# Kernel tuning notes

Measured on AMD Instinct MI355X. Metric: run time of the kernel, lower is better.

The kernel has to match this reference:

```python
import jax, jax.numpy as jnp
import numpy as np

N_REF = 4

def setup_inputs() -> dict:
    key = jax.random.key(0)
    ks = jax.random.split(key, 6)
    B, C, H, W = 4, 256, 64, 64
    s = 1.0 / np.sqrt(C)
    return {
        'x': jax.random.normal(ks[0], (B, C, H, W), jnp.float32),
        'Wq': jax.random.normal(ks[1], (C, C), jnp.float32) * s,
        'bq': jnp.zeros((C,), jnp.float32),
        'Wk': jax.random.normal(ks[2], (C, C), jnp.float32) * s,
        'bk': jnp.zeros((C,), jnp.float32),
        'Wv': jax.random.normal(ks[3], (C, C), jnp.float32) * s,
        'bv': jnp.zeros((C,), jnp.float32),
        'Woff': jax.random.normal(ks[4], (2 * N_REF, C), jnp.float32) * s,
        'boff': jnp.zeros((2 * N_REF,), jnp.float32),
    }

def _proj(x, W, b):
    # 1x1 conv == channel-mixing linear: [B,C,H,W] -> [B,O,H,W]
    return jnp.einsum('oc,bchw->bohw', W, x) + b[None, :, None, None]

def reference(x, Wq, bq, Wk, bk, Wv, bv, Woff, boff):
    B, C, H, W = x.shape
    n = N_REF
    HW = H * W
    Q = _proj(x, Wq, bq)
    K = _proj(x, Wk, bk)
    V = _proj(x, Wv, bv)
    offsets = _proj(Q, Woff, boff).reshape(B, n, 2, H, W)
    grid_h, grid_w = jnp.meshgrid(jnp.arange(H), jnp.arange(W), indexing='ij')
    ref_x = jnp.clip(jnp.round(grid_w[None, None] + offsets[:, :, 0]).astype(jnp.int32), 0, W - 1)
    ref_y = jnp.clip(jnp.round(grid_h[None, None] + offsets[:, :, 1]).astype(jnp.int32), 0, H - 1)
    ref_idx = (ref_y * W + ref_x).reshape(B, n, HW)          # [B,n,HW]
    K_flat = K.reshape(B, C, HW)
    V_flat = V.reshape(B, C, HW)
    # gather along spatial dim -> [B,C,n,HW]
    idx = ref_idx[:, None, :, :]                              # [B,1,n,HW]
    K_g = jnp.take_along_axis(K_flat[:, :, None, :], idx, axis=3)
    V_g = jnp.take_along_axis(V_flat[:, :, None, :], idx, axis=3)
    Q_flat = Q.reshape(B, C, HW)
    attn = jnp.einsum('bch,bcnh->bnh', Q_flat, K_g)
    attn = jax.nn.softmax(attn, axis=1)
    out = jnp.einsum('bnh,bcnh->bch', attn, V_g)
    return out.reshape(B, C, H, W)
```

## Files before the change

### kernel.cpp

```cpp
#include <hip/hip_runtime.h>
#include <math.h>

#define B_DIM   4
#define C_DIM   256
#define H_DIM   64
#define W_DIM   64
#define HW_DIM  4096
#define NPIX    (B_DIM * HW_DIM)
#define NREF    4

typedef unsigned short u16;
typedef __attribute__((ext_vector_type(4))) unsigned short u16x4;
typedef __attribute__((ext_vector_type(8))) unsigned short u16x8;
typedef __attribute__((ext_vector_type(8))) short bf16x8;
typedef __attribute__((ext_vector_type(4))) float f32x4;

__device__ __forceinline__ u16 bf16_rne(float f) {
    unsigned u = __float_as_uint(f);
    u = u + 0x7FFFu + ((u >> 16) & 1u);
    return (u16)(u >> 16);
}
__device__ __forceinline__ float bf16_tof(u16 h) {
    return __uint_as_float(((unsigned)h) << 16);
}
__device__ __forceinline__ void gload16(const void* g, void* l) {
    __builtin_amdgcn_global_load_lds(
        (const __attribute__((address_space(1))) void*)g,
        (__attribute__((address_space(3))) void*)l, 16, 0, 0);
}

__global__ __launch_bounds__(256) void prep_kernel(
    const float* __restrict__ Wq, const float* __restrict__ bq,
    const float* __restrict__ Woff, const float* __restrict__ boff,
    const float* __restrict__ Wk, const float* __restrict__ Wv,
    double* __restrict__ Weffp, double* __restrict__ beff,
    u16* __restrict__ Bswh, u16* __restrict__ Bswl)
{
    const int bx = blockIdx.x;
    const int t  = threadIdx.x;

    if (bx < 32) {
        const int j  = bx >> 2;
        const int q  = bx & 3;
        const int o0 = q * 64;
        double s0 = 0, s1 = 0, s2 = 0, s3 = 0;
        for (int o = o0; o < o0 + 64; o += 4) {
            s0 += (double)Woff[j * C_DIM + o + 0] * (double)Wq[(size_t)(o + 0) * C_DIM + t];
            s1 += (double)Woff[j * C_DIM + o + 1] * (double)Wq[(size_t)(o + 1) * C_DIM + t];
            s2 += (double)Woff[j * C_DIM + o + 2] * (double)Wq[(size_t)(o + 2) * C_DIM + t];
            s3 += (double)Woff[j * C_DIM + o + 3] * (double)Wq[(size_t)(o + 3) * C_DIM + t];
        }
        Weffp[(size_t)(q * 8 + j) * C_DIM + t] = (s0 + s1) + (s2 + s3);

        if (q == 0) {
            __shared__ double red[256];
            red[t] = (double)Woff[j * C_DIM + t] * (double)bq[t];
            __syncthreads();
            for (int st = 128; st > 0; st >>= 1) {
                if (t < st) red[t] += red[t + st];
                __syncthreads();
            }
            if (t == 0) beff[j] = red[0] + (double)boff[j];
        }
    } else {
        const int T     = bx - 32;
        const int kt    = T & 3;
        const int ntile = (T >> 2) & 1;
        const int mat   = T >> 3;
        const float* Wm = (mat == 0) ? Wq : (mat == 1) ? Wk : Wv;
        const int n0 = ntile * 128, k0 = kt * 64;
        u16* dh = Bswh + (size_t)T * 8192;
        u16* dl = Bswl + (size_t)T * 8192;
#pragma unroll
        for (int it = 0; it < 4; ++it) {
            const int s   = it * 256 + t;
            const int row = s >> 3;
            const int ch  = s & 7;
            const int kk  = k0 + (ch ^ (row & 7)) * 8;
            const float4 w0 = *(const float4*)(Wm + (size_t)(n0 + row) * C_DIM + kk);
            const float4 w1 = *(const float4*)(Wm + (size_t)(n0 + row) * C_DIM + kk + 4);
            u16x8 hv, lv;
            hv[0] = bf16_rne(w0.x); lv[0] = bf16_rne(w0.x - bf16_tof(hv[0]));
            hv[1] = bf16_rne(w0.y); lv[1] = bf16_rne(w0.y - bf16_tof(hv[1]));
            hv[2] = bf16_rne(w0.z); lv[2] = bf16_rne(w0.z - bf16_tof(hv[2]));
            hv[3] = bf16_rne(w0.w); lv[3] = bf16_rne(w0.w - bf16_tof(hv[3]));
            hv[4] = bf16_rne(w1.x); lv[4] = bf16_rne(w1.x - bf16_tof(hv[4]));
            hv[5] = bf16_rne(w1.y); lv[5] = bf16_rne(w1.y - bf16_tof(hv[5]));
            hv[6] = bf16_rne(w1.z); lv[6] = bf16_rne(w1.z - bf16_tof(hv[6]));
            hv[7] = bf16_rne(w1.w); lv[7] = bf16_rne(w1.w - bf16_tof(hv[7]));
            *(u16x8*)(dh + (size_t)s * 8) = hv;
            *(u16x8*)(dl + (size_t)s * 8) = lv;
        }
    }
}

__global__ __launch_bounds__(256) void xsplit_kernel(
    const float* __restrict__ x, const double* __restrict__ Weffp,
    u16* __restrict__ xh, u16* __restrict__ xl, double* __restrict__ part)
{
    __shared__ float  tile[64][65];
    __shared__ double wf[8][64];
    const int b   = blockIdx.z;
    const int cy  = blockIdx.y;
    const int c0  = cy * 64;
    const int hw0 = blockIdx.x * 64;
    const int t   = threadIdx.x;
    const int r4  = t >> 6;
    const int col = t & 63;

#pragma unroll
    for (int i = 0; i < 16; ++i) {
        const int row = i * 4 + r4;
        tile[row][col] = x[((size_t)b * C_DIM + c0 + row) * HW_DIM + hw0 + col];
    }
#pragma unroll
    for (int d = t; d < 512; d += 256) {
        const int jj = d >> 6, cc = d & 63;
        ((double*)wf)[d] = Weffp[(size_t)(0 + jj) * C_DIM + c0 + cc]
                         + Weffp[(size_t)(8 + jj) * C_DIM + c0 + cc]
                         + Weffp[(size_t)(16 + jj) * C_DIM + c0 + cc]
                         + Weffp[(size_t)(24 + jj) * C_DIM + c0 + cc];
    }
    __syncthreads();

#pragma unroll
    for (int i = 0; i < 16; ++i) {
        const int hwr = i * 4 + r4;
        const float v = tile[col][hwr];
        const u16 h = bf16_rne(v);
        const float lo = v - bf16_tof(h);
        const size_t o = ((size_t)b * HW_DIM + hw0 + hwr) * C_DIM + c0 + col;
        xh[o] = h;
        xl[o] = bf16_rne(lo);
    }

    const int p = col, g = r4;
    double a0 = 0, a1 = 0;
    for (int c = 0; c < 64; ++c) {
        const double xv = (double)tile[c][p];
        a0 += wf[2 * g][c] * xv;
        a1 += wf[2 * g + 1][c] * xv;
    }
    const int pix = b * HW_DIM + hw0 + p;
    part[(size_t)(cy * 8 + 2 * g) * NPIX + pix]     = a0;
    part[(size_t)(cy * 8 + 2 * g + 1) * NPIX + pix] = a1;
}

__global__ __launch_bounds__(256) void idx_kernel(
    const double* __restrict__ part, const double* __restrict__ beff,
    int* __restrict__ idx_buf)
{
    const int pix = blockIdx.x * 256 + threadIdx.x;
    const int hw  = pix & (HW_DIM - 1);
    const int h   = hw >> 6;
    const int w   = hw & 63;

    double o[8];
#pragma unroll
    for (int j = 0; j < 8; ++j)
        o[j] = part[(size_t)(0 + j) * NPIX + pix] + part[(size_t)(8 + j) * NPIX + pix]
             + part[(size_t)(16 + j) * NPIX + pix] + part[(size_t)(24 + j) * NPIX + pix]
             + beff[j];

    int r[NREF];
#pragma unroll
    for (int n = 0; n < NREF; ++n) {
        const float ox = (float)o[2 * n];
        const float oy = (float)o[2 * n + 1];
        int rx = (int)rintf((float)w + ox);
        int ry = (int)rintf((float)h + oy);
        rx = min(max(rx, 0), W_DIM - 1);
        ry = min(max(ry, 0), H_DIM - 1);
        r[n] = ry * W_DIM + rx;
    }
    int4 outv; outv.x = r[0]; outv.y = r[1]; outv.z = r[2]; outv.w = r[3];
    *(int4*)(idx_buf + (size_t)pix * 4) = outv;
}

__global__ __launch_bounds__(256) void qkv_mfma(
    const u16* __restrict__ xh, const u16* __restrict__ xl,
    const u16* __restrict__ Bswh, const u16* __restrict__ Bswl,
    const float* __restrict__ bq, const float* __restrict__ bk,
    const float* __restrict__ bv,
    float* __restrict__ Qt, float* __restrict__ Kt, float* __restrict__ Vt)
{
    const int mat   = blockIdx.z;
    const int ntile = blockIdx.y;
    const int m0    = blockIdx.x * 64;
    const int n0    = ntile * 128;
    const bool three = (mat != 2);
    const float* bm = (mat == 0) ? bq : (mat == 1) ? bk : bv;
    float*      Out = (mat == 0) ? Qt : (mat == 1) ? Kt : Vt;

    __shared__ u16 lds[24576];
    u16* Ah = lds;
    u16* Al = lds + 4096;
    u16* Bh = lds + 8192;
    u16* Bl = lds + 16384;

    const int t    = threadIdx.x;
    const int lane = t & 63;
    const int wv   = t >> 6;
    const int wm   = (wv >> 1) * 32;
    const int wn   = (wv & 1) * 64;

    f32x4 acc[2][4] = {};

    for (int kt = 0; kt < 4; ++kt) {
        const int k0 = kt * 64;
        const size_t Tb = (size_t)((mat * 2 + ntile) * 4 + kt) * 8192;

#pragma unroll
        for (int it = 0; it < 2; ++it) {
            const int s   = it * 256 + t;
            const int row = s >> 3;
            const int sch = (s & 7) ^ (row & 7);
            const size_t goff = (size_t)(m0 + row) * C_DIM + k0 + sch * 8;
            gload16(xh + goff, (char*)Ah + s * 16);
            if (three) gload16(xl + goff, (char*)Al + s * 16);
        }
#pragma unroll
        for (int it = 0; it < 4; ++it) {
            const int s = it * 256 + t;
            gload16(Bswh + Tb + (size_t)s * 8, (char*)Bh + s * 16);
            if (three) gload16(Bswl + Tb + (size_t)s * 8, (char*)Bl + s * 16);
        }
        __syncthreads();

#pragma unroll
        for (int ks = 0; ks < 2; ++ks) {
            bf16x8 afh[2], afl[2], bfh[4], bfl[4];
#pragma unroll
            for (int mt = 0; mt < 2; ++mt) {
                const int row = wm + mt * 16 + (lane & 15);
                const int ch  = (ks * 4 + (lane >> 4)) ^ (row & 7);
                const int off = row * 128 + ch * 16;
                afh[mt] = *(const bf16x8*)((const char*)Ah + off);
                if (three) afl[mt] = *(const bf16x8*)((const char*)Al + off);
            }
#pragma unroll
            for (int nt = 0; nt < 4; ++nt) {
                const int row = wn + nt * 16 + (lane & 15);
                const int ch  = (ks * 4 + (lane >> 4)) ^ (row & 7);
                const int off = row * 128 + ch * 16;
                bfh[nt] = *(const bf16x8*)((const char*)Bh + off);
                if (three) bfl[nt] = *(const bf16x8*)((const char*)Bl + off);
            }
#pragma unroll
            for (int mt = 0; mt < 2; ++mt)
#pragma unroll
                for (int nt = 0; nt < 4; ++nt) {
                    acc[mt][nt] = __builtin_amdgcn_mfma_f32_16x16x32_bf16(afh[mt], bfh[nt], acc[mt][nt], 0, 0, 0);
                    if (three) {
                        acc[mt][nt] = __builtin_amdgcn_mfma_f32_16x16x32_bf16(afh[mt], bfl[nt], acc[mt][nt], 0, 0, 0);
                        acc[mt][nt] = __builtin_amdgcn_mfma_f32_16x16x32_bf16(afl[mt], bfh[nt], acc[mt][nt], 0, 0, 0);
                    }
                }
        }
        __syncthreads();
    }

    const int col = lane & 15;
    const int rg  = (lane >> 4) * 4;
#pragma unroll
    for (int nt = 0; nt < 4; ++nt) {
        const int n = n0 + wn + nt * 16 + col;
        const float bias = bm[n];
#pragma unroll
        for (int mt = 0; mt < 2; ++mt) {
            const int m = m0 + wm + mt * 16 + rg;
#pragma unroll
            for (int r = 0; r < 4; ++r)
                Out[(size_t)(m + r) * C_DIM + n] = acc[mt][nt][r] + bias;
        }
    }
}

__global__ __launch_bounds__(1024) void attn_kernel(
    const float* __restrict__ Qt,
    const float* __restrict__ Kt,
    const float* __restrict__ Vt,
    const int*   __restrict__ idx_buf,
    float* __restrict__ out)
{
    __shared__ float trans[16][260];

    const int t    = threadIdx.x;
    const int wave = t >> 6;
    const int lane = t & 63;

    const int pix0 = blockIdx.x * 16;
    const int b    = pix0 / HW_DIM;
    const int hw   = (pix0 % HW_DIM) + wave;
    const int pix  = b * HW_DIM + hw;

    const float* qrow = Qt + (size_t)pix * C_DIM;
    float q[4];
    *(float4*)q = *(const float4*)(qrow + lane * 4);

    const int4 iv = *(const int4*)(idx_buf + (size_t)pix * 4);
    int idx[NREF] = {iv.x, iv.y, iv.z, iv.w};

    float logit[NREF];
#pragma unroll
    for (int n = 0; n < NREF; ++n) {
        const float* krow = Kt + ((size_t)b * HW_DIM + idx[n]) * C_DIM;
        float4 kv = *(const float4*)(krow + lane * 4);
        float lp = fmaf(q[3], kv.w, fmaf(q[2], kv.z, fmaf(q[1], kv.y, q[0] * kv.x)));
#pragma unroll
        for (int off = 1; off < 64; off <<= 1) lp += __shfl_xor(lp, off);
        logit[n] = lp;
    }

    float mx = fmaxf(fmaxf(logit[0], logit[1]), fmaxf(logit[2], logit[3]));
    float e[NREF], s = 0.0f;
#pragma unroll
    for (int n = 0; n < NREF; ++n) { e[n] = expf(logit[n] - mx); s += e[n]; }
    float wgt[NREF];
#pragma unroll
    for (int n = 0; n < NREF; ++n) wgt[n] = e[n] / s;

    float o4[4] = {0.f, 0.f, 0.f, 0.f};
#pragma unroll
    for (int n = 0; n < NREF; ++n) {
        const float* vrow = Vt + ((size_t)b * HW_DIM + idx[n]) * C_DIM;
        float4 vv = *(const float4*)(vrow + lane * 4);
        o4[0] = fmaf(wgt[n], vv.x, o4[0]);
        o4[1] = fmaf(wgt[n], vv.y, o4[1]);
        o4[2] = fmaf(wgt[n], vv.z, o4[2]);
        o4[3] = fmaf(wgt[n], vv.w, o4[3]);
    }

    *(float4*)&trans[wave][lane * 4] = *(float4*)o4;
    __syncthreads();

    float* ob = out + (size_t)b * C_DIM * HW_DIM + (pix0 % HW_DIM);
    const int px = t & 15;
#pragma unroll
    for (int cc = 0; cc < C_DIM; cc += 64) {
        const int c = cc + (t >> 4);
        ob[(size_t)c * HW_DIM + px] = trans[px][c];
    }
}

extern "C" void kernel_launch(void* const* d_in, const int* in_sizes, int n_in,
                              void* d_out, int out_size, void* d_ws, size_t ws_size,
                              hipStream_t stream) {
    const float* x    = (const float*)d_in[0];
    const float* Wq   = (const float*)d_in[1];
    const float* bq   = (const float*)d_in[2];
    const float* Wk   = (const float*)d_in[3];
    const float* bk   = (const float*)d_in[4];
    const float* Wv   = (const float*)d_in[5];
    const float* bv   = (const float*)d_in[6];
    const float* Woff = (const float*)d_in[7];
    const float* boff = (const float*)d_in[8];
    float* out = (float*)d_out;

    char* ws = (char*)d_ws;
    float*  Kt    = (float*)ws;
    float*  Vt    = (float*)(ws + (size_t)16 * 1024 * 1024);
    float*  Qt    = (float*)(ws + (size_t)32 * 1024 * 1024);
    u16*    xh    = (u16*)  (ws + (size_t)48 * 1024 * 1024);
    u16*    xl    = (u16*)  (ws + (size_t)56 * 1024 * 1024);
    char*   aux   = ws + (size_t)64 * 1024 * 1024;
    double* Weffp = (double*)(aux);
    double* beff  = (double*)(aux + 64 * 1024);
    int*    idxb  = (int*)   (aux + 128 * 1024);
    u16*    Bswh  = (u16*)   (aux + 512 * 1024);
    u16*    Bswl  = (u16*)   (aux + 1024 * 1024);
    double* part  = (double*)(aux + 2 * 1024 * 1024);

    prep_kernel<<<dim3(56), dim3(256), 0, stream>>>(
        Wq, bq, Woff, boff, Wk, Wv, Weffp, beff, Bswh, Bswl);
    xsplit_kernel<<<dim3(HW_DIM / 64, C_DIM / 64, B_DIM), dim3(256), 0, stream>>>(
        x, Weffp, xh, xl, part);
    idx_kernel<<<dim3(NPIX / 256), dim3(256), 0, stream>>>(part, beff, idxb);
    qkv_mfma<<<dim3(NPIX / 64, 2, 3), dim3(256), 0, stream>>>(
        xh, xl, Bswh, Bswl, bq, bk, bv, Qt, Kt, Vt);
    attn_kernel<<<dim3(NPIX / 16), dim3(1024), 0, stream>>>(
        Qt, Kt, Vt, idxb, out);
}
```

Baseline: 62.79 us.

## Fold Wq into K projection to eliminate the Q GEMM

```diff
diff --git a/kernel.cpp b/kernel.cpp
--- a/kernel.cpp
+++ b/kernel.cpp
@@ -8,6 +8,7 @@
 #define HW_DIM  4096
 #define NPIX    (B_DIM * HW_DIM)
 #define NREF    4
+#define NJ      10
 
 typedef unsigned short u16;
 typedef __attribute__((ext_vector_type(4))) unsigned short u16x4;
@@ -29,68 +30,95 @@
         (__attribute__((address_space(3))) void*)l, 16, 0, 0);
 }
 
-__global__ __launch_bounds__(256) void prep_kernel(
+__global__ __launch_bounds__(256) void prep1_kernel(
     const float* __restrict__ Wq, const float* __restrict__ bq,
+    const float* __restrict__ Wk, const float* __restrict__ bk,
     const float* __restrict__ Woff, const float* __restrict__ boff,
-    const float* __restrict__ Wk, const float* __restrict__ Wv,
     double* __restrict__ Weffp, double* __restrict__ beff,
-    u16* __restrict__ Bswh, u16* __restrict__ Bswl)
+    double* __restrict__ Mt)
 {
     const int bx = blockIdx.x;
     const int t  = threadIdx.x;
 
-    if (bx < 32) {
+    if (bx < 4 * NJ) {
         const int j  = bx >> 2;
         const int q  = bx & 3;
         const int o0 = q * 64;
+        const float* Avec = (j < 8) ? (Woff + j * C_DIM) : ((j == 8) ? bq : bk);
+        const float* Bmat = (j == 8) ? Wk : Wq;
         double s0 = 0, s1 = 0, s2 = 0, s3 = 0;
         for (int o = o0; o < o0 + 64; o += 4) {
-            s0 += (double)Woff[j * C_DIM + o + 0] * (double)Wq[(size_t)(o + 0) * C_DIM + t];
-            s1 += (double)Woff[j * C_DIM + o + 1] * (double)Wq[(size_t)(o + 1) * C_DIM + t];
-            s2 += (double)Woff[j * C_DIM + o + 2] * (double)Wq[(size_t)(o + 2) * C_DIM + t];
-            s3 += (double)Woff[j * C_DIM + o + 3] * (double)Wq[(size_t)(o + 3) * C_DIM + t];
-        }
-        Weffp[(size_t)(q * 8 + j) * C_DIM + t] = (s0 + s1) + (s2 + s3);
-
-        if (q == 0) {
+            s0 += (double)Avec[o + 0] * (double)Bmat[(size_t)(o + 0) * C_DIM + t];
+            s1 += (double)Avec[o + 1] * (double)Bmat[(size_t)(o + 1) * C_DIM + t];
+            s2 += (double)Avec[o + 2] * (double)Bmat[(size_t)(o + 2) * C_DIM + t];
+            s3 += (double)Avec[o + 3] * (double)Bmat[(size_t)(o + 3) * C_DIM + t];
+        }
+        Weffp[(size_t)(q * NJ + j) * C_DIM + t] = (s0 + s1) + (s2 + s3);
+
+        if (q == 0 && j <= 8) {
             __shared__ double red[256];
-            red[t] = (double)Woff[j * C_DIM + t] * (double)bq[t];
+            red[t] = (j < 8) ? (double)Woff[j * C_DIM + t] * (double)bq[t]
+                             : (double)bq[t] * (double)bk[t];
             __syncthreads();
             for (int st = 128; st > 0; st >>= 1) {
                 if (t < st) red[t] += red[t + st];
                 __syncthreads();
             }
-            if (t == 0) beff[j] = red[0] + (double)boff[j];
+            if (t == 0) beff[j] = (j < 8) ? red[0] + (double)boff[j] : red[0];
         }
     } else {
-        const int T     = bx - 32;
-        const int kt    = T & 3;
-        const int ntile = (T >> 2) & 1;
-        const int mat   = T >> 3;
-        const float* Wm = (mat == 0) ? Wq : (mat == 1) ? Wk : Wv;
-        const int n0 = ntile * 128, k0 = kt * 64;
-        u16* dh = Bswh + (size_t)T * 8192;
-        u16* dl = Bswl + (size_t)T * 8192;
-#pragma unroll
-        for (int it = 0; it < 4; ++it) {
-            const int s   = it * 256 + t;
-            const int row = s >> 3;
-            const int ch  = s & 7;
-            const int kk  = k0 + (ch ^ (row & 7)) * 8;
-            const float4 w0 = *(const float4*)(Wm + (size_t)(n0 + row) * C_DIM + kk);
-            const float4 w1 = *(const float4*)(Wm + (size_t)(n0 + row) * C_DIM + kk + 4);
-            u16x8 hv, lv;
-            hv[0] = bf16_rne(w0.x); lv[0] = bf16_rne(w0.x - bf16_tof(hv[0]));
-            hv[1] = bf16_rne(w0.y); lv[1] = bf16_rne(w0.y - bf16_tof(hv[1]));
-            hv[2] = bf16_rne(w0.z); lv[2] = bf16_rne(w0.z - bf16_tof(hv[2]));
-            hv[3] = bf16_rne(w0.w); lv[3] = bf16_rne(w0.w - bf16_tof(hv[3]));
-            hv[4] = bf16_rne(w1.x); lv[4] = bf16_rne(w1.x - bf16_tof(hv[4]));
-            hv[5] = bf16_rne(w1.y); lv[5] = bf16_rne(w1.y - bf16_tof(hv[5]));
-            hv[6] = bf16_rne(w1.z); lv[6] = bf16_rne(w1.z - bf16_tof(hv[6]));
-            hv[7] = bf16_rne(w1.w); lv[7] = bf16_rne(w1.w - bf16_tof(hv[7]));
-            *(u16x8*)(dh + (size_t)s * 8) = hv;
-            *(u16x8*)(dl + (size_t)s * 8) = lv;
-        }
+        const int c = bx - 4 * NJ;
+        __shared__ float wqcol[256];
+        wqcol[t] = Wq[(size_t)t * C_DIM + c];
+        __syncthreads();
+        double a0 = 0, a1 = 0, a2 = 0, a3 = 0;
+        for (int o = 0; o < C_DIM; o += 4) {
+            a0 += (double)wqcol[o + 0] * (double)Wk[(size_t)(o + 0) * C_DIM + t];
+            a1 += (double)wqcol[o + 1] * (double)Wk[(size_t)(o + 1) * C_DIM + t];
+            a2 += (double)wqcol[o + 2] * (double)Wk[(size_t)(o + 2) * C_DIM + t];
+            a3 += (double)wqcol[o + 3] * (double)Wk[(size_t)(o + 3) * C_DIM + t];
+        }
+        Mt[(size_t)c * C_DIM + t] = (a0 + a1) + (a2 + a3);
+    }
+}
+
+__global__ __launch_bounds__(256) void prep2_kernel(
+    const double* __restrict__ Mt, const float* __restrict__ Wv,
+    u16* __restrict__ Bswh, u16* __restrict__ Bswl)
+{
+    const int T     = blockIdx.x;
+    const int kt    = T & 3;
+    const int ntile = (T >> 2) & 1;
+    const int mat   = T >> 3;
+    const int n0 = ntile * 128, k0 = kt * 64;
+    const int t  = threadIdx.x;
+    u16* dh = Bswh + (size_t)T * 8192;
+    u16* dl = Bswl + (size_t)T * 8192;
+
+#pragma unroll
+    for (int it = 0; it < 4; ++it) {
+        const int s   = it * 256 + t;
+        const int row = s >> 3;
+        const int ch  = s & 7;
+        const int kk  = k0 + (ch ^ (row & 7)) * 8;
+        float v[8];
+        if (mat == 0) {
+            const double* src = Mt + (size_t)(n0 + row) * C_DIM + kk;
+#pragma unroll
+            for (int i = 0; i < 8; ++i) v[i] = (float)src[i];
+        } else {
+            const float* src = Wv + (size_t)(n0 + row) * C_DIM + kk;
+#pragma unroll
+            for (int i = 0; i < 8; ++i) v[i] = src[i];
+        }
+        u16x8 hv, lv;
+#pragma unroll
+        for (int i = 0; i < 8; ++i) {
+            hv[i] = bf16_rne(v[i]);
+            lv[i] = bf16_rne(v[i] - bf16_tof(hv[i]));
+        }
+        *(u16x8*)(dh + (size_t)s * 8) = hv;
+        if (mat == 0) *(u16x8*)(dl + (size_t)s * 8) = lv;
     }
 }
 
@@ -99,7 +127,7 @@
     u16* __restrict__ xh, u16* __restrict__ xl, double* __restrict__ part)
 {
     __shared__ float  tile[64][65];
-    __shared__ double wf[8][64];
+    __shared__ double wf[NJ][64];
     const int b   = blockIdx.z;
     const int cy  = blockIdx.y;
     const int c0  = cy * 64;
@@ -113,13 +141,12 @@
         const int row = i * 4 + r4;
         tile[row][col] = x[((size_t)b * C_DIM + c0 + row) * HW_DIM + hw0 + col];
     }
-#pragma unroll
-    for (int d = t; d < 512; d += 256) {
+    for (int d = t; d < NJ * 64; d += 256) {
         const int jj = d >> 6, cc = d & 63;
-        ((double*)wf)[d] = Weffp[(size_t)(0 + jj) * C_DIM + c0 + cc]
-                         + Weffp[(size_t)(8 + jj) * C_DIM + c0 + cc]
-                         + Weffp[(size_t)(16 + jj) * C_DIM + c0 + cc]
-                         + Weffp[(size_t)(24 + jj) * C_DIM + c0 + cc];
+        ((double*)wf)[d] = Weffp[(size_t)(0 * NJ + jj) * C_DIM + c0 + cc]
+                         + Weffp[(size_t)(1 * NJ + jj) * C_DIM + c0 + cc]
+                         + Weffp[(size_t)(2 * NJ + jj) * C_DIM + c0 + cc]
+                         + Weffp[(size_t)(3 * NJ + jj) * C_DIM + c0 + cc];
     }
     __syncthreads();
 
@@ -135,20 +162,22 @@
     }
 
     const int p = col, g = r4;
-    double a0 = 0, a1 = 0;
+    double a0 = 0, a1 = 0, a2 = 0;
     for (int c = 0; c < 64; ++c) {
         const double xv = (double)tile[c][p];
         a0 += wf[2 * g][c] * xv;
         a1 += wf[2 * g + 1][c] * xv;
+        if (g < 2) a2 += wf[8 + g][c] * xv;
     }
     const int pix = b * HW_DIM + hw0 + p;
-    part[(size_t)(cy * 8 + 2 * g) * NPIX + pix]     = a0;
-    part[(size_t)(cy * 8 + 2 * g + 1) * NPIX + pix] = a1;
+    part[(size_t)(cy * NJ + 2 * g) * NPIX + pix]     = a0;
+    part[(size_t)(cy * NJ + 2 * g + 1) * NPIX + pix] = a1;
+    if (g < 2) part[(size_t)(cy * NJ + 8 + g) * NPIX + pix] = a2;
 }
 
 __global__ __launch_bounds__(256) void idx_kernel(
     const double* __restrict__ part, const double* __restrict__ beff,
-    int* __restrict__ idx_buf)
+    int* __restrict__ idx_buf, float* __restrict__ kqf, float* __restrict__ vqf)
 {
     const int pix = blockIdx.x * 256 + threadIdx.x;
     const int hw  = pix & (HW_DIM - 1);
@@ -158,8 +187,8 @@
     double o[8];
 #pragma unroll
     for (int j = 0; j < 8; ++j)
-        o[j] = part[(size_t)(0 + j) * NPIX + pix] + part[(size_t)(8 + j) * NPIX + pix]
-             + part[(size_t)(16 + j) * NPIX + pix] + part[(size_t)(24 + j) * NPIX + pix]
+        o[j] = part[(size_t)(0 * NJ + j) * NPIX + pix] + part[(size_t)(1 * NJ + j) * NPIX + pix]
+             + part[(size_t)(2 * NJ + j) * NPIX + pix] + part[(size_t)(3 * NJ + j) * NPIX + pix]
              + beff[j];
 
     int r[NREF];
@@ -175,22 +204,28 @@
     }
     int4 outv; outv.x = r[0]; outv.y = r[1]; outv.z = r[2]; outv.w = r[3];
     *(int4*)(idx_buf + (size_t)pix * 4) = outv;
+
+    const double kq = part[(size_t)(0 * NJ + 8) * NPIX + pix] + part[(size_t)(1 * NJ + 8) * NPIX + pix]
+                    + part[(size_t)(2 * NJ + 8) * NPIX + pix] + part[(size_t)(3 * NJ + 8) * NPIX + pix];
+    const double vq = part[(size_t)(0 * NJ + 9) * NPIX + pix] + part[(size_t)(1 * NJ + 9) * NPIX + pix]
+                    + part[(size_t)(2 * NJ + 9) * NPIX + pix] + part[(size_t)(3 * NJ + 9) * NPIX + pix]
+                    + beff[8];
+    kqf[pix] = (float)kq;
+    vqf[pix] = (float)vq;
 }
 
 __global__ __launch_bounds__(256) void qkv_mfma(
     const u16* __restrict__ xh, const u16* __restrict__ xl,
     const u16* __restrict__ Bswh, const u16* __restrict__ Bswl,
-    const float* __restrict__ bq, const float* __restrict__ bk,
     const float* __restrict__ bv,
-    float* __restrict__ Qt, float* __restrict__ Kt, float* __restrict__ Vt)
+    float* __restrict__ Kpt, float* __restrict__ Vt)
 {
     const int mat   = blockIdx.z;
     const int ntile = blockIdx.y;
     const int m0    = blockIdx.x * 64;
     const int n0    = ntile * 128;
-    const bool three = (mat != 2);
-    const float* bm = (mat == 0) ? bq : (mat == 1) ? bk : bv;
-    float*      Out = (mat == 0) ? Qt : (mat == 1) ? Kt : Vt;
+    const bool three = (mat == 0);
+    float* Out = mat ? Vt : Kpt;
 
     __shared__ u16 lds[24576];
     u16* Ah = lds;
@@ -265,7 +300,7 @@
 #pragma unroll
     for (int nt = 0; nt < 4; ++nt) {
         const int n = n0 + wn + nt * 16 + col;
-        const float bias = bm[n];
+        const float bias = mat ? bv[n] : 0.0f;
 #pragma unroll
         for (int mt = 0; mt < 2; ++mt) {
             const int m = m0 + wm + mt * 16 + rg;
@@ -277,10 +312,13 @@
 }
 
 __global__ __launch_bounds__(1024) void attn_kernel(
-    const float* __restrict__ Qt,
-    const float* __restrict__ Kt,
+    const u16*   __restrict__ xh,
+    const u16*   __restrict__ xl,
+    const float* __restrict__ Kpt,
     const float* __restrict__ Vt,
     const int*   __restrict__ idx_buf,
+    const float* __restrict__ kqf,
+    const float* __restrict__ vqf,
     float* __restrict__ out)
 {
     __shared__ float trans[16][260];
@@ -294,22 +332,25 @@
     const int hw   = (pix0 % HW_DIM) + wave;
     const int pix  = b * HW_DIM + hw;
 
-    const float* qrow = Qt + (size_t)pix * C_DIM;
+    const u16x4 hv = *(const u16x4*)(xh + (size_t)pix * C_DIM + lane * 4);
+    const u16x4 lv = *(const u16x4*)(xl + (size_t)pix * C_DIM + lane * 4);
     float q[4];
-    *(float4*)q = *(const float4*)(qrow + lane * 4);
+#pragma unroll
+    for (int i = 0; i < 4; ++i) q[i] = bf16_tof(hv[i]) + bf16_tof(lv[i]);
 
     const int4 iv = *(const int4*)(idx_buf + (size_t)pix * 4);
     int idx[NREF] = {iv.x, iv.y, iv.z, iv.w};
+    const float vq = vqf[pix];
 
     float logit[NREF];
 #pragma unroll
     for (int n = 0; n < NREF; ++n) {
-        const float* krow = Kt + ((size_t)b * HW_DIM + idx[n]) * C_DIM;
+        const float* krow = Kpt + ((size_t)b * HW_DIM + idx[n]) * C_DIM;
         float4 kv = *(const float4*)(krow + lane * 4);
         float lp = fmaf(q[3], kv.w, fmaf(q[2], kv.z, fmaf(q[1], kv.y, q[0] * kv.x)));
 #pragma unroll
         for (int off = 1; off < 64; off <<= 1) lp += __shfl_xor(lp, off);
-        logit[n] = lp;
+        logit[n] = lp + kqf[(size_t)b * HW_DIM + idx[n]] + vq;
     }
 
     float mx = fmaxf(fmaxf(logit[0], logit[1]), fmaxf(logit[2], logit[3]));
@@ -358,26 +399,29 @@
     float* out = (float*)d_out;
 
     char* ws = (char*)d_ws;
-    float*  Kt    = (float*)ws;
+    float*  Kpt   = (float*)ws;
     float*  Vt    = (float*)(ws + (size_t)16 * 1024 * 1024);
-    float*  Qt    = (float*)(ws + (size_t)32 * 1024 * 1024);
     u16*    xh    = (u16*)  (ws + (size_t)48 * 1024 * 1024);
     u16*    xl    = (u16*)  (ws + (size_t)56 * 1024 * 1024);
     char*   aux   = ws + (size_t)64 * 1024 * 1024;
     double* Weffp = (double*)(aux);
-    double* beff  = (double*)(aux + 64 * 1024);
-    int*    idxb  = (int*)   (aux + 128 * 1024);
-    u16*    Bswh  = (u16*)   (aux + 512 * 1024);
-    u16*    Bswl  = (u16*)   (aux + 1024 * 1024);
+    double* beff  = (double*)(aux + 128 * 1024);
+    int*    idxb  = (int*)   (aux + 192 * 1024);
+    float*  kqf   = (float*) (aux + 448 * 1024);
+    float*  vqf   = (float*) (aux + 512 * 1024);
+    u16*    Bswh  = (u16*)   (aux + 576 * 1024);
+    u16*    Bswl  = (u16*)   (aux + 832 * 1024);
+    double* Mt    = (double*)(aux + 1088 * 1024);
     double* part  = (double*)(aux + 2 * 1024 * 1024);
 
-    prep_kernel<<<dim3(56), dim3(256), 0, stream>>>(
-        Wq, bq, Woff, boff, Wk, Wv, Weffp, beff, Bswh, Bswl);
+    prep1_kernel<<<dim3(4 * NJ + 256), dim3(256), 0, stream>>>(
+        Wq, bq, Wk, bk, Woff, boff, Weffp, beff, Mt);
+    prep2_kernel<<<dim3(16), dim3(256), 0, stream>>>(Mt, Wv, Bswh, Bswl);
     xsplit_kernel<<<dim3(HW_DIM / 64, C_DIM / 64, B_DIM), dim3(256), 0, stream>>>(
         x, Weffp, xh, xl, part);
-    idx_kernel<<<dim3(NPIX / 256), dim3(256), 0, stream>>>(part, beff, idxb);
-    qkv_mfma<<<dim3(NPIX / 64, 2, 3), dim3(256), 0, stream>>>(
-        xh, xl, Bswh, Bswl, bq, bk, bv, Qt, Kt, Vt);
+    idx_kernel<<<dim3(NPIX / 256), dim3(256), 0, stream>>>(part, beff, idxb, kqf, vqf);
+    qkv_mfma<<<dim3(NPIX / 64, 2, 2), dim3(256), 0, stream>>>(
+        xh, xl, Bswh, Bswl, bv, Kpt, Vt);
     attn_kernel<<<dim3(NPIX / 16), dim3(1024), 0, stream>>>(
-        Qt, Kt, Vt, idxb, out);
-}
+        xh, xl, Kpt, Vt, idxb, kqf, vqf, out);
+}
```

Result: slower. 69.71 us (+11.0%).
